# Performance work log

Measured on AMD Instinct MI355X. Metric: run time of the kernel, lower is better.

Reference implementation:

```python
import jax, jax.numpy as jnp
import numpy as np
import math

P_PARTICLES = 50
N_ITERS = 30
ROT_RANGE = math.radians(45.0)
TR_RANGE = 1.0
F_DE = 0.8
CR_DE = 0.9
SUB = 128


def axis_angle_to_rotation_matrix(v):
    # v: [..., 3] axis-angle -> [..., 3, 3] via Rodrigues formula
    theta = jnp.linalg.norm(v, axis=-1, keepdims=True)            # [..., 1]
    k = v / jnp.maximum(theta, 1e-8)
    kx, ky, kz = k[..., 0], k[..., 1], k[..., 2]
    zero = jnp.zeros_like(kx)
    K = jnp.stack([zero, -kz, ky,
                   kz, zero, -kx,
                   -ky, kx, zero], axis=-1).reshape(v.shape[:-1] + (3, 3))
    I = jnp.eye(3, dtype=v.dtype)
    s = jnp.sin(theta)[..., None]
    c = jnp.cos(theta)[..., None]
    R = I + s * K + (1.0 - c) * (K @ K)
    return jnp.where(theta[..., None] < 1e-8, I, R)


def _evaluate(src, tgt, pop):
    # src: [B,S,3] subsampled source, tgt: [B,S,3], pop: [B,P,6]
    R = axis_angle_to_rotation_matrix(pop[..., :3])               # [B,P,3,3]
    t = pop[..., 3:]                                              # [B,P,3]
    # transformed[b,p,n,k] = sum_j src[b,n,j] * R[b,p,k,j] + t[b,p,k]
    x = jnp.einsum('bnj,bpkj->bpnk', src, R) + t[:, :, None, :]   # [B,P,S,3]
    # squared-distance chamfer (symmetric, mean of nearest-neighbor dists)
    xn = jnp.sum(x * x, axis=-1)                                  # [B,P,S]
    yn = jnp.sum(tgt * tgt, axis=-1)                              # [B,S]
    cross = jnp.einsum('bpnd,bmd->bpnm', x, tgt)                  # [B,P,S,S]
    d2 = jnp.maximum(xn[..., None] + yn[:, None, None, :] - 2.0 * cross, 0.0)
    return d2.min(axis=-1).mean(axis=-1) + d2.min(axis=-2).mean(axis=-1)  # [B,P]


def setup_inputs() -> dict:
    key = jax.random.key(0)
    k1, k2 = jax.random.split(key)
    source = jax.random.normal(k1, (32, 16384, 3), dtype=jnp.float32)
    target = jax.random.normal(k2, (32, 16384, 3), dtype=jnp.float32)
    return {"source": source, "target": target}


def reference(source, target):
    B, N, _ = source.shape
    M = target.shape[1]
    P = P_PARTICLES
    key = jax.random.key(42)
    k0, k1, k2, k3, kloop = jax.random.split(key, 5)

    # subsample points for fitness evaluation (shared indices across batch)
    idx_s = jax.random.permutation(k0, N)[:SUB]
    idx_t = jax.random.permutation(k1, M)[:SUB]
    src = source[:, idx_s, :]                                     # [B,S,3]
    tgt = target[:, idx_t, :]                                     # [B,S,3]

    # init population: uniform axis-angle + translation; particle 0 = identity
    rot = jax.random.uniform(k2, (B, P, 3), minval=-ROT_RANGE, maxval=ROT_RANGE)
    tr = jax.random.uniform(k3, (B, P, 3), minval=-TR_RANGE, maxval=TR_RANGE)
    pop = jnp.concatenate([rot, tr], axis=-1).at[:, 0, :].set(0.0)
    fit = _evaluate(src, tgt, pop)                                # [B,P]

    dim_ids = jnp.arange(6)

    def step(carry, k):
        pop, fit = carry
        ka, kb, kc = jax.random.split(k, 3)
        # per-batch random permutations of particle indices (r1, r2, r3)
        perm_keys = jax.random.split(ka, 3 * B)
        perms = jax.vmap(lambda kk: jax.random.permutation(kk, P))(perm_keys)
        perms = perms.reshape(3, B, P)

        def gather(r):
            return jnp.take_along_axis(pop, r[..., None], axis=1)  # [B,P,6]

        x1, x2, x3 = gather(perms[0]), gather(perms[1]), gather(perms[2])
        mutant = x1 + F_DE * (x2 - x3)
        mutant = jnp.concatenate([
            jnp.clip(mutant[..., :3], -ROT_RANGE, ROT_RANGE),
            jnp.clip(mutant[..., 3:], -TR_RANGE, TR_RANGE),
        ], axis=-1)

        rmask = jax.random.uniform(kb, (B, P, 6)) < CR_DE
        j_rand = jax.random.randint(kc, (B, P), 0, 6)
        cross_mask = rmask | (dim_ids == j_rand[..., None])
        trial = jnp.where(cross_mask, mutant, pop)

        tfit = _evaluate(src, tgt, trial)
        improved = tfit < fit
        pop = jnp.where(improved[..., None], trial, pop)
        fit = jnp.where(improved, tfit, fit)
        return (pop, fit), None

    (pop, fit), _ = jax.lax.scan(step, (pop, fit), jax.random.split(kloop, N_ITERS))

    best_idx = jnp.argmin(fit, axis=1)                            # [B]
    best_pos = pop[jnp.arange(B), best_idx]                       # [B,6]
    R_best = axis_angle_to_rotation_matrix(best_pos[:, :3])       # [B,3,3]
    t_best = best_pos[:, 3:]                                      # [B,3]
    aligned = jnp.einsum('bnj,bkj->bnk', source, R_best) + t_best[:, None, :]
    return (R_best, t_best, aligned)
```

## Files before the change

### kernel.cpp

```cpp
#include <hip/hip_runtime.h>
#include <stdint.h>

struct U2 { unsigned a, b; };

__device__ __forceinline__ unsigned rotl32(unsigned v, int r) {
  return (v << r) | (v >> (32 - r));
}

__device__ __forceinline__ U2 tf(U2 k, unsigned x0, unsigned x1) {
  unsigned ks0 = k.a, ks1 = k.b, ks2 = k.a ^ k.b ^ 0x1BD11BDAu;
  x0 += ks0; x1 += ks1;
#define TFG(RA, RB, RC, RD, KA, KB, INC)                  \
  x0 += x1; x1 = rotl32(x1, RA); x1 ^= x0;                \
  x0 += x1; x1 = rotl32(x1, RB); x1 ^= x0;                \
  x0 += x1; x1 = rotl32(x1, RC); x1 ^= x0;                \
  x0 += x1; x1 = rotl32(x1, RD); x1 ^= x0;                \
  x0 += KA; x1 += KB + INC;
  TFG(13, 15, 26, 6, ks1, ks2, 1u)
  TFG(17, 29, 16, 24, ks2, ks0, 2u)
  TFG(13, 15, 26, 6, ks0, ks1, 3u)
  TFG(17, 29, 16, 24, ks1, ks2, 4u)
  TFG(13, 15, 26, 6, ks2, ks0, 5u)
#undef TFG
  U2 r; r.a = x0; r.b = x1; return r;
}

__device__ __forceinline__ U2 split_key(U2 key, int num, int j) {
  (void)num;
  return tf(key, 0u, (unsigned)j);
}
__device__ __forceinline__ unsigned random_bits(U2 key, int n, unsigned e) {
  (void)n;
  U2 r = tf(key, 0u, e);
  return r.a ^ r.b;
}

__device__ __forceinline__ U2 root_key() { U2 k; k.a = 0u; k.b = 42u; return k; }

__device__ __forceinline__ float jax_uniform(U2 key, int n, unsigned e,
                                             float minv, float maxv) {
  unsigned b = random_bits(key, n, e);
  float u = __uint_as_float((b >> 9) | 0x3f800000u) - 1.0f;
  float r = u * (maxv - minv) + minv;
  return fmaxf(minv, r);
}

#define ROTR 0.7853981633974483f

__device__ __forceinline__ void compute_R(float vx, float vy, float vz,
                                          float R[3][3]) {
  float nsq = vx * vx + vy * vy + vz * vz;
  float theta = sqrtf(nsq);
  if (theta < 1e-8f) {
    R[0][0] = 1.f; R[0][1] = 0.f; R[0][2] = 0.f;
    R[1][0] = 0.f; R[1][1] = 1.f; R[1][2] = 0.f;
    R[2][0] = 0.f; R[2][1] = 0.f; R[2][2] = 1.f;
    return;
  }
  float m = fmaxf(theta, 1e-8f);
  float kx = vx / m, ky = vy / m, kz = vz / m;
  float s = sinf(theta), c = cosf(theta);
  float K[3][3] = {{0.f, -kz, ky}, {kz, 0.f, -kx}, {-ky, kx, 0.f}};
  float K2[3][3];
#pragma unroll
  for (int i = 0; i < 3; i++)
#pragma unroll
    for (int j = 0; j < 3; j++)
      K2[i][j] = fmaf(K[i][2], K[2][j], fmaf(K[i][1], K[1][j], K[i][0] * K[0][j]));
  float omc = 1.0f - c;
#pragma unroll
  for (int i = 0; i < 3; i++)
#pragma unroll
    for (int j = 0; j < 3; j++)
      R[i][j] = ((i == j) ? 1.0f : 0.0f) + s * K[i][j] + omc * K2[i][j];
}

__device__ __forceinline__ unsigned long long make_composite(int s, int i) {
  U2 root = root_key();
  U2 kp = split_key(root, 5, s >> 1);
  U2 key;
  if ((s & 1) == 0) {
    key = split_key(kp, 2, 1);
  } else {
    U2 kA = split_key(kp, 2, 0);
    key = split_key(kA, 2, 1);
  }
  unsigned rb = random_bits(key, 16384, (unsigned)i);
  return ((unsigned long long)rb << 32) | (unsigned)i;
}

__device__ __forceinline__ float gload(const float* p) {
  return __hip_atomic_load(const_cast<float*>(p), __ATOMIC_RELAXED,
                           __HIP_MEMORY_SCOPE_AGENT);
}
__device__ __forceinline__ void gstore(float* p, float v) {
  __hip_atomic_store(p, v, __ATOMIC_RELAXED, __HIP_MEMORY_SCOPE_AGENT);
}
__device__ __forceinline__ unsigned uload(const unsigned* p) {
  return __hip_atomic_load(const_cast<unsigned*>(p), __ATOMIC_RELAXED,
                           __HIP_MEMORY_SCOPE_AGENT);
}
__device__ __forceinline__ void ustore(unsigned* p, unsigned v) {
  __hip_atomic_store(p, v, __ATOMIC_RELAXED, __HIP_MEMORY_SCOPE_AGENT);
}

__global__ __launch_bounds__(256) void hist_kernel(unsigned* __restrict__ hist) {
  int gid = blockIdx.x * 256 + threadIdx.x;
  int s = gid >> 14, i = gid & 16383;
  unsigned long long c = make_composite(s, i);
  unsigned bucket = (unsigned)(c >> 56);
  atomicAdd(&hist[s * 256 + bucket], 1u);
}

__global__ __launch_bounds__(256) void prefix_kernel(
    const unsigned* __restrict__ hist, unsigned* __restrict__ base,
    unsigned* __restrict__ cursor) {
  __shared__ unsigned h[4][256];
  int t = threadIdx.x;
#pragma unroll
  for (int s = 0; s < 4; s++) h[s][t] = hist[s * 256 + t];
  __syncthreads();
#pragma unroll
  for (int s = 0; s < 4; s++) {
    unsigned acc = 0;
    for (int j = 0; j < 256; j++) acc += (j < t) ? h[s][j] : 0u;
    base[s * 256 + t] = acc;
    cursor[s * 256 + t] = acc;
  }
}

__global__ __launch_bounds__(256) void scatterb_kernel(
    unsigned* __restrict__ cursor, unsigned long long* __restrict__ sorted) {
  int gid = blockIdx.x * 256 + threadIdx.x;
  int s = gid >> 14, i = gid & 16383;
  unsigned long long c = make_composite(s, i);
  unsigned bucket = (unsigned)(c >> 56);
  unsigned pos = atomicAdd(&cursor[s * 256 + bucket], 1u);
  sorted[(s << 14) + pos] = c;
}

__global__ __launch_bounds__(256) void rank_kernel(
    const unsigned long long* __restrict__ sorted,
    const unsigned* __restrict__ base, const unsigned* __restrict__ hist,
    unsigned* __restrict__ rank_all, unsigned* __restrict__ x1buf) {
  int gid = blockIdx.x * 256 + threadIdx.x;
  int s = gid >> 14, k = gid & 16383;
  unsigned long long c = sorted[(s << 14) + k];
  unsigned bucket = (unsigned)(c >> 56);
  unsigned b0 = base[s * 256 + bucket];
  unsigned cnt = hist[s * 256 + bucket];
  unsigned less = 0;
  for (unsigned j = 0; j < cnt; j++)
    less += (sorted[(s << 14) + b0 + j] < c) ? 1u : 0u;
  unsigned i = (unsigned)(c & 0xffffffffull);
  unsigned rank = b0 + less;
  if ((s & 1) == 0) x1buf[((s >> 1) << 14) + rank] = i;
  else              rank_all[(s << 14) + i] = rank;
}

__global__ __launch_bounds__(256) void idx_kernel(
    const unsigned* __restrict__ rank_all, const unsigned* __restrict__ x1buf,
    int* __restrict__ idx) {
  int gid = blockIdx.x * 256 + threadIdx.x;
  int perm = gid >> 14, i = gid & 16383;
  unsigned r = rank_all[((perm * 2 + 1) << 14) + i];
  if (r < 128u) idx[perm * 128 + (int)r] = (int)x1buf[(perm << 14) + i];
}

__global__ __launch_bounds__(128) void setupperm_kernel(
    const float* __restrict__ source, const float* __restrict__ target,
    const int* __restrict__ idx, float* __restrict__ src,
    float* __restrict__ tgt, float* __restrict__ yn,
    unsigned* __restrict__ packg) {
  int blk = blockIdx.x;
  int tid = threadIdx.x;
  if (blk < 32) {
    int b = blk;
    int is = idx[tid], it = idx[128 + tid];
#pragma unroll
    for (int d = 0; d < 3; d++)
      src[(b * 128 + tid) * 3 + d] = source[((size_t)b * 16384 + is) * 3 + d];
    float y0 = target[((size_t)b * 16384 + it) * 3 + 0];
    float y1 = target[((size_t)b * 16384 + it) * 3 + 1];
    float y2 = target[((size_t)b * 16384 + it) * 3 + 2];
    tgt[(b * 128 + tid) * 3 + 0] = y0;
    tgt[(b * 128 + tid) * 3 + 1] = y1;
    tgt[(b * 128 + tid) * 3 + 2] = y2;
    yn[b * 128 + tid] = y0 * y0 + y1 * y1 + y2 * y2;
    return;
  }
  int blk2 = blk - 32;
  int it = blk2 >> 5, b = blk2 & 31;
  __shared__ unsigned pbits[3][64];
  __shared__ int lperm[3][64];
  U2 root = root_key();
  U2 kloop = split_key(root, 5, 4);
  U2 kit = split_key(kloop, 30, it);
  U2 ka = split_key(kit, 3, 0);
  for (int e = tid; e < 150; e += 128) {
    int r = e / 50, q = e % 50;
    U2 pk = split_key(ka, 96, r * 32 + b);
    U2 sub = split_key(pk, 2, 1);
    pbits[r][q] = random_bits(sub, 50, (unsigned)q);
  }
  __syncthreads();
  for (int e = tid; e < 150; e += 128) {
    int r = e / 50, q = e % 50;
    unsigned bq = pbits[r][q];
    int cnt = 0;
    for (int j = 0; j < 50; j++) {
      unsigned bj = pbits[r][j];
      cnt += (bj < bq || (bj == bq && j < q)) ? 1 : 0;
    }
    lperm[r][cnt] = q;
  }
  __syncthreads();
  if (tid < 50) {
    int p = tid, bp = b * 50 + p;
    U2 kb = split_key(kit, 3, 1);
    U2 kc = split_key(kit, 3, 2);
    U2 kc1 = split_key(kc, 2, 0), kc2 = split_key(kc, 2, 1);
    unsigned hb = random_bits(kc1, 1600, (unsigned)bp);
    unsigned lb = random_bits(kc2, 1600, (unsigned)bp);
    int jr = (int)((((hb % 6u) * 4u) + (lb % 6u)) % 6u);
    unsigned mask = 0;
#pragma unroll
    for (int d = 0; d < 6; d++) {
      unsigned rb = random_bits(kb, 9600, (unsigned)(bp * 6 + d));
      float u = __uint_as_float((rb >> 9) | 0x3f800000u) - 1.0f;
      if ((u < 0.9f) || (d == jr)) mask |= (1u << d);
    }
    unsigned pack = (unsigned)lperm[0][p] | ((unsigned)lperm[1][p] << 6) |
                    ((unsigned)lperm[2][p] << 12) | (mask << 18);
    packg[(it * 32 + b) * 50 + p] = pack;
  }
}

__device__ __forceinline__ float eval_pose_core(
    float p0, float p1, float p2, float p3, float p4, float p5,
    float s0, float s1, float s2, int tid, const float4* syv, float4* xsv,
    float* rowpart, float* red1, float* red2) {
  float Rm[3][3];
  compute_R(p0, p1, p2, Rm);
  float x0 = fmaf(Rm[0][2], s2, fmaf(Rm[0][1], s1, Rm[0][0] * s0)) + p3;
  float x1 = fmaf(Rm[1][2], s2, fmaf(Rm[1][1], s1, Rm[1][0] * s0)) + p4;
  float x2 = fmaf(Rm[2][2], s2, fmaf(Rm[2][1], s1, Rm[2][0] * s0)) + p5;
  float xn = x0 * x0 + x1 * x1 + x2 * x2;
  xsv[tid] = make_float4(x0, x1, x2, xn);
  __syncthreads();
  int rg = tid & 31, cq = tid >> 5;
  float4 xr0 = xsv[4 * rg + 0];
  float4 xr1 = xsv[4 * rg + 1];
  float4 xr2 = xsv[4 * rg + 2];
  float4 xr3 = xsv[4 * rg + 3];
  float racc0 = 3.402823466e38f, racc1 = 3.402823466e38f;
  float racc2 = 3.402823466e38f, racc3 = 3.402823466e38f;
  float cacc[32];
#pragma unroll
  for (int cj = 0; cj < 32; cj++) {
    float4 y = syv[(cq << 5) + cj];
    float cr0 = fmaf(xr0.z, y.z, fmaf(xr0.y, y.y, xr0.x * y.x));
    float d0 = (xr0.w + y.w) - 2.0f * cr0; d0 = fmaxf(d0, 0.0f);
    float cr1 = fmaf(xr1.z, y.z, fmaf(xr1.y, y.y, xr1.x * y.x));
    float d1 = (xr1.w + y.w) - 2.0f * cr1; d1 = fmaxf(d1, 0.0f);
    float cr2 = fmaf(xr2.z, y.z, fmaf(xr2.y, y.y, xr2.x * y.x));
    float d2_ = (xr2.w + y.w) - 2.0f * cr2; d2_ = fmaxf(d2_, 0.0f);
    float cr3 = fmaf(xr3.z, y.z, fmaf(xr3.y, y.y, xr3.x * y.x));
    float d3 = (xr3.w + y.w) - 2.0f * cr3; d3 = fmaxf(d3, 0.0f);
    racc0 = fminf(racc0, d0); racc1 = fminf(racc1, d1);
    racc2 = fminf(racc2, d2_); racc3 = fminf(racc3, d3);
    cacc[cj] = fminf(fminf(d0, d1), fminf(d2_, d3));
  }
  rowpart[cq * 128 + 4 * rg + 0] = racc0;
  rowpart[cq * 128 + 4 * rg + 1] = racc1;
  rowpart[cq * 128 + 4 * rg + 2] = racc2;
  rowpart[cq * 128 + 4 * rg + 3] = racc3;
#pragma unroll
  for (int m = 16; m >= 1; m >>= 1) {
    bool hi = (rg & m) != 0;
#pragma unroll
    for (int j = 0; j < m; j++) {
      float lo_v = cacc[j], hi_v = cacc[j + m];
      float mine = hi ? hi_v : lo_v;
      float send = hi ? lo_v : hi_v;
      float recv = __shfl_xor(send, m, 64);
      cacc[j] = fminf(mine, recv);
    }
  }
  float colmin = cacc[0];
  __syncthreads();
  float rv = rowpart[tid];
  rv = fminf(rv, rowpart[128 + tid]);
  rv = fminf(rv, rowpart[256 + tid]);
  rv = fminf(rv, rowpart[384 + tid]);
  red1[tid] = rv;
  red2[tid] = colmin;
  __syncthreads();
  int l = tid & 63;
  float v1 = red1[l] + red1[l + 64];
  float v2 = red2[l] + red2[l + 64];
#pragma unroll
  for (int m = 32; m >= 1; m >>= 1) {
    v1 += __shfl_xor(v1, m, 64);
    v2 += __shfl_xor(v2, m, 64);
  }
  return v1 * 0.0078125f + v2 * 0.0078125f;
}

__device__ __forceinline__ float pop0_val(int b, int r, int d) {
  if (r == 0) return 0.0f;
  U2 root = root_key();
  unsigned ridx = (unsigned)((b * 50 + r) * 3 + (d % 3));
  if (d < 3) {
    U2 k2 = split_key(root, 5, 2);
    return jax_uniform(k2, 4800, ridx, -ROTR, ROTR);
  }
  U2 k3 = split_key(root, 5, 3);
  return jax_uniform(k3, 4800, ridx, -1.0f, 1.0f);
}

__global__ __launch_bounds__(128, 4) void de_loop_kernel(
    const float* __restrict__ srcb, const float* __restrict__ tgtb,
    const float* __restrict__ ynb, const unsigned* __restrict__ packg,
    float* __restrict__ estate, unsigned* __restrict__ flags,
    const float* __restrict__ source, float* __restrict__ out) {
  int blk = blockIdx.x;
  int b = blk / 50, p = blk % 50;
  int bp = blk;
  int tid = threadIdx.x;
  __shared__ float strial[8];
  __shared__ float pv4[4][6];
  __shared__ float4 syv[128];
  __shared__ float4 xsv[128];
  __shared__ float rowpart[512];
  __shared__ float red1[128];
  __shared__ float red2[128];
  __shared__ float fl[52];
  __shared__ float Rsh2[12];

  {
    float y0 = tgtb[(b * 128 + tid) * 3 + 0];
    float y1 = tgtb[(b * 128 + tid) * 3 + 1];
    float y2 = tgtb[(b * 128 + tid) * 3 + 2];
    syv[tid] = make_float4(y0, y1, y2, ynb[b * 128 + tid]);
  }
  float s0 = srcb[(b * 128 + tid) * 3 + 0];
  float s1 = srcb[(b * 128 + tid) * 3 + 1];
  float s2 = srcb[(b * 128 + tid) * 3 + 2];

  float own_f = 0.0f;
  float own_e = 0.0f;

  for (int it = 0; it < 30; it++) {
    unsigned pack = packg[(it * 32 + b) * 50 + p];
    int i1 = (int)(pack & 63u);
    int i2 = (int)((pack >> 6) & 63u);
    int i3 = (int)((pack >> 12) & 63u);
    unsigned mask = (pack >> 18) & 63u;

    if (it == 0) {
      if (tid < 24) {
        int u = tid / 6, d = tid % 6;
        int rows[4] = {p, i1, i2, i3};
        pv4[u][d] = pop0_val(b, rows[u], d);
      }
      __syncthreads();
      float f0 = eval_pose_core(pv4[0][0], pv4[0][1], pv4[0][2], pv4[0][3],
                                pv4[0][4], pv4[0][5],
                                s0, s1, s2, tid, syv, xsv, rowpart, red1, red2);
      if (tid < 6) {
        int d = tid;
        float mu = pv4[1][d] + 0.8f * (pv4[2][d] - pv4[3][d]);
        if (d < 3) mu = fminf(fmaxf(mu, -ROTR), ROTR);
        else       mu = fminf(fmaxf(mu, -1.0f), 1.0f);
        float pv = pv4[0][d];
        float tv = ((mask >> d) & 1u) ? mu : pv;
        strial[d] = tv;
      }
      __syncthreads();
      float tf0 = eval_pose_core(strial[0], strial[1], strial[2], strial[3],
                                 strial[4], strial[5],
                                 s0, s1, s2, tid, syv, xsv, rowpart, red1, red2);
      bool imp = tf0 < f0;
      own_f = imp ? tf0 : f0;
      if (tid < 6) own_e = imp ? strial[tid] : pv4[0][tid];
    } else {
      if (tid < 3) {
        int dq = (tid == 0) ? i1 : (tid == 1) ? i2 : i3;
        const unsigned* fp = &flags[(b * 50 + dq) * 16];
        while (uload(fp) < (unsigned)it) __builtin_amdgcn_s_sleep(1);
      }
      __syncthreads();
      if (tid < 6) {
        int d = tid;
        const float* eb = &estate[((size_t)(it - 1) * 1600 + b * 50) * 8];
        float x1v = gload(&eb[i1 * 8 + d]);
        float x2v = gload(&eb[i2 * 8 + d]);
        float x3v = gload(&eb[i3 * 8 + d]);
        float mu = x1v + 0.8f * (x2v - x3v);
        if (d < 3) mu = fminf(fmaxf(mu, -ROTR), ROTR);
        else       mu = fminf(fmaxf(mu, -1.0f), 1.0f);
        float tv = ((mask >> d) & 1u) ? mu : own_e;
        strial[d] = tv;
      }
      __syncthreads();
      float tfv = eval_pose_core(strial[0], strial[1], strial[2], strial[3],
                                 strial[4], strial[5],
                                 s0, s1, s2, tid, syv, xsv, rowpart, red1, red2);
      bool imp = tfv < own_f;
      own_f = imp ? tfv : own_f;
      if (tid < 6) own_e = imp ? strial[tid] : own_e;
    }

    float* slot = &estate[((size_t)it * 1600 + bp) * 8];
    if (tid < 6) gstore(&slot[tid], own_e);
    if (tid == 6) gstore(&slot[6], own_f);
    __syncthreads();
    if (tid == 0) ustore(&flags[bp * 16], (unsigned)(it + 1));
  }

  if (tid < 50) {
    const unsigned* fp = &flags[(b * 50 + tid) * 16];
    while (uload(fp) < 30u) __builtin_amdgcn_s_sleep(1);
    fl[tid] = gload(&estate[((size_t)29 * 1600 + b * 50 + tid) * 8 + 6]);
  }
  __syncthreads();
  if (tid == 0) {
    int bi = 0;
    float best = fl[0];
    for (int q = 1; q < 50; q++)
      if (fl[q] < best) { best = fl[q]; bi = q; }
    const float* ep = &estate[((size_t)29 * 1600 + b * 50 + bi) * 8];
    float v[6];
#pragma unroll
    for (int d = 0; d < 6; d++) v[d] = gload(&ep[d]);
    float R[3][3];
    compute_R(v[0], v[1], v[2], R);
#pragma unroll
    for (int i = 0; i < 3; i++)
#pragma unroll
      for (int j = 0; j < 3; j++) Rsh2[i * 3 + j] = R[i][j];
    Rsh2[9] = v[3]; Rsh2[10] = v[4]; Rsh2[11] = v[5];
    if (p == 0) {
#pragma unroll
      for (int e = 0; e < 9; e++) out[b * 9 + e] = Rsh2[e];
      out[288 + b * 3 + 0] = v[3];
      out[288 + b * 3 + 1] = v[4];
      out[288 + b * 3 + 2] = v[5];
    }
  }
  __syncthreads();

  for (int k = p * 128 + tid; k < 16384; k += 6400) {
    size_t gid = (size_t)b * 16384 + k;
    float a0s = source[gid * 3 + 0];
    float a1s = source[gid * 3 + 1];
    float a2s = source[gid * 3 + 2];
    float a0 = fmaf(Rsh2[2], a2s, fmaf(Rsh2[1], a1s, Rsh2[0] * a0s)) + Rsh2[9];
    float a1 = fmaf(Rsh2[5], a2s, fmaf(Rsh2[4], a1s, Rsh2[3] * a0s)) + Rsh2[10];
    float a2 = fmaf(Rsh2[8], a2s, fmaf(Rsh2[7], a1s, Rsh2[6] * a0s)) + Rsh2[11];
    out[384 + gid * 3 + 0] = a0;
    out[384 + gid * 3 + 1] = a1;
    out[384 + gid * 3 + 2] = a2;
  }
}

extern "C" void kernel_launch(void* const* d_in, const int* in_sizes, int n_in,
                              void* d_out, int out_size, void* d_ws,
                              size_t ws_size, hipStream_t stream) {
  const float* source = (const float*)d_in[0];
  const float* target = (const float*)d_in[1];
  float* out = (float*)d_out;
  char* ws = (char*)d_ws;

  unsigned* packg    = (unsigned*)(ws + 0);
  float* srcb        = (float*)(ws + 192000);
  float* tgtb        = (float*)(ws + 241152);
  float* ynb         = (float*)(ws + 290304);
  int* idx           = (int*)(ws + 306688);
  unsigned* hist     = (unsigned*)(ws + 307712);
  unsigned* flags    = (unsigned*)(ws + 311808);
  unsigned* basep    = (unsigned*)(ws + 414208);
  unsigned* cursor   = (unsigned*)(ws + 418304);
  unsigned long long* sorted = (unsigned long long*)(ws + 422400);
  unsigned* rank_all = (unsigned*)(ws + 946688);
  unsigned* x1buf    = (unsigned*)(ws + 1208832);
  float* estate      = (float*)(ws + 422400);

  hipMemsetAsync(hist, 0, 106496, stream);
  hist_kernel<<<256, 256, 0, stream>>>(hist);
  prefix_kernel<<<1, 256, 0, stream>>>(hist, basep, cursor);
  scatterb_kernel<<<256, 256, 0, stream>>>(cursor, sorted);
  rank_kernel<<<256, 256, 0, stream>>>(sorted, basep, hist, rank_all, x1buf);
  idx_kernel<<<128, 256, 0, stream>>>(rank_all, x1buf, idx);
  setupperm_kernel<<<992, 128, 0, stream>>>(source, target, idx, srcb, tgtb,
                                            ynb, packg);

  de_loop_kernel<<<1600, 128, 0, stream>>>(srcb, tgtb, ynb, packg, estate,
                                           flags, source, out);
}
```

Baseline: 362.4 us.

## Replace per-block ready flags with sentinel-valued state polling

Removes the separate flags array and its barrier-plus-flag publish step. The DE state buffer is instead pre-filled with 0xFFFFFFFF sentinels, and consumers spin directly on the data words until every needed value is non-sentinel. The next iteration's permutation pack is also prefetched one step ahead. This cuts one __syncthreads and a flag round-trip per iteration, in exchange for an extra memset of the state buffer and tight spinning without sleep. It also depends on no valid float ever having the sentinel bit pattern and on each word being visible as it is written.

```diff
diff --git a/kernel.cpp b/kernel.cpp
--- a/kernel.cpp
+++ b/kernel.cpp
@@ -46,6 +46,7 @@
 }
 
 #define ROTR 0.7853981633974483f
+#define SENTINEL 0xFFFFFFFFu
 
 __device__ __forceinline__ void compute_R(float vx, float vy, float vz,
                                           float R[3][3]) {
@@ -100,8 +101,12 @@
   return __hip_atomic_load(const_cast<unsigned*>(p), __ATOMIC_RELAXED,
                            __HIP_MEMORY_SCOPE_AGENT);
 }
-__device__ __forceinline__ void ustore(unsigned* p, unsigned v) {
-  __hip_atomic_store(p, v, __ATOMIC_RELAXED, __HIP_MEMORY_SCOPE_AGENT);
+
+__device__ __forceinline__ float poll_word(const float* p) {
+  const unsigned* up = (const unsigned*)p;
+  unsigned v = uload(up);
+  while (v == SENTINEL) v = uload(up);
+  return __uint_as_float(v);
 }
 
 __global__ __launch_bounds__(256) void hist_kernel(unsigned* __restrict__ hist) {
@@ -322,8 +327,8 @@
 __global__ __launch_bounds__(128, 4) void de_loop_kernel(
     const float* __restrict__ srcb, const float* __restrict__ tgtb,
     const float* __restrict__ ynb, const unsigned* __restrict__ packg,
-    float* __restrict__ estate, unsigned* __restrict__ flags,
-    const float* __restrict__ source, float* __restrict__ out) {
+    float* __restrict__ estate, const float* __restrict__ source,
+    float* __restrict__ out) {
   int blk = blockIdx.x;
   int b = blk / 50, p = blk % 50;
   int bp = blk;
@@ -351,8 +356,11 @@
   float own_f = 0.0f;
   float own_e = 0.0f;
 
+  unsigned pack_next = packg[(0 * 32 + b) * 50 + p];
+
   for (int it = 0; it < 30; it++) {
-    unsigned pack = packg[(it * 32 + b) * 50 + p];
+    unsigned pack = pack_next;
+    if (it < 29) pack_next = packg[((it + 1) * 32 + b) * 50 + p];
     int i1 = (int)(pack & 63u);
     int i2 = (int)((pack >> 6) & 63u);
     int i3 = (int)((pack >> 12) & 63u);
@@ -385,18 +393,19 @@
       own_f = imp ? tf0 : f0;
       if (tid < 6) own_e = imp ? strial[tid] : pv4[0][tid];
     } else {
-      if (tid < 3) {
-        int dq = (tid == 0) ? i1 : (tid == 1) ? i2 : i3;
-        const unsigned* fp = &flags[(b * 50 + dq) * 16];
-        while (uload(fp) < (unsigned)it) __builtin_amdgcn_s_sleep(1);
-      }
-      __syncthreads();
       if (tid < 6) {
         int d = tid;
         const float* eb = &estate[((size_t)(it - 1) * 1600 + b * 50) * 8];
-        float x1v = gload(&eb[i1 * 8 + d]);
-        float x2v = gload(&eb[i2 * 8 + d]);
-        float x3v = gload(&eb[i3 * 8 + d]);
+        const unsigned* pa = (const unsigned*)&eb[i1 * 8 + d];
+        const unsigned* pb = (const unsigned*)&eb[i2 * 8 + d];
+        const unsigned* pc = (const unsigned*)&eb[i3 * 8 + d];
+        unsigned va = uload(pa), vb = uload(pb), vc = uload(pc);
+        while (va == SENTINEL || vb == SENTINEL || vc == SENTINEL) {
+          va = uload(pa); vb = uload(pb); vc = uload(pc);
+        }
+        float x1v = __uint_as_float(va);
+        float x2v = __uint_as_float(vb);
+        float x3v = __uint_as_float(vc);
         float mu = x1v + 0.8f * (x2v - x3v);
         if (d < 3) mu = fminf(fmaxf(mu, -ROTR), ROTR);
         else       mu = fminf(fmaxf(mu, -1.0f), 1.0f);
@@ -413,16 +422,12 @@
     }
 
     float* slot = &estate[((size_t)it * 1600 + bp) * 8];
-    if (tid < 6) gstore(&slot[tid], own_e);
-    if (tid == 6) gstore(&slot[6], own_f);
-    __syncthreads();
-    if (tid == 0) ustore(&flags[bp * 16], (unsigned)(it + 1));
+    if (tid < 6)       gstore(&slot[tid], own_e);
+    else if (tid == 6) gstore(&slot[6], own_f);
   }
 
   if (tid < 50) {
-    const unsigned* fp = &flags[(b * 50 + tid) * 16];
-    while (uload(fp) < 30u) __builtin_amdgcn_s_sleep(1);
-    fl[tid] = gload(&estate[((size_t)29 * 1600 + b * 50 + tid) * 8 + 6]);
+    fl[tid] = poll_word(&estate[((size_t)29 * 1600 + b * 50 + tid) * 8 + 6]);
   }
   __syncthreads();
   if (tid == 0) {
@@ -433,7 +438,7 @@
     const float* ep = &estate[((size_t)29 * 1600 + b * 50 + bi) * 8];
     float v[6];
 #pragma unroll
-    for (int d = 0; d < 6; d++) v[d] = gload(&ep[d]);
+    for (int d = 0; d < 6; d++) v[d] = poll_word(&ep[d]);
     float R[3][3];
     compute_R(v[0], v[1], v[2], R);
 #pragma unroll
@@ -479,7 +484,6 @@
   float* ynb         = (float*)(ws + 290304);
   int* idx           = (int*)(ws + 306688);
   unsigned* hist     = (unsigned*)(ws + 307712);
-  unsigned* flags    = (unsigned*)(ws + 311808);
   unsigned* basep    = (unsigned*)(ws + 414208);
   unsigned* cursor   = (unsigned*)(ws + 418304);
   unsigned long long* sorted = (unsigned long long*)(ws + 422400);
@@ -487,15 +491,16 @@
   unsigned* x1buf    = (unsigned*)(ws + 1208832);
   float* estate      = (float*)(ws + 422400);
 
-  hipMemsetAsync(hist, 0, 106496, stream);
+  hipMemsetAsync(hist, 0, 4096, stream);
   hist_kernel<<<256, 256, 0, stream>>>(hist);
   prefix_kernel<<<1, 256, 0, stream>>>(hist, basep, cursor);
   scatterb_kernel<<<256, 256, 0, stream>>>(cursor, sorted);
   rank_kernel<<<256, 256, 0, stream>>>(sorted, basep, hist, rank_all, x1buf);
   idx_kernel<<<128, 256, 0, stream>>>(rank_all, x1buf, idx);
+  hipMemsetAsync(estate, 0xFF, 1536000, stream);
   setupperm_kernel<<<992, 128, 0, stream>>>(source, target, idx, srcb, tgtb,
                                             ynb, packg);
 
   de_loop_kernel<<<1600, 128, 0, stream>>>(srcb, tgtb, ynb, packg, estate,
-                                           flags, source, out);
-}
+                                           source, out);
+}
```

Result: no change. 362.4 us (-0.0%).
